# Optimization experiments

Hardware: AMD Instinct MI355X
Metric: run time of the kernel (lower is better)

The kernel has to match this reference:

```python
import jax, jax.numpy as jnp
import numpy as np


def _unfold(x, k, pad, stride):
    # torch.nn.functional.unfold: [B,C,H,W] -> [B, C*k*k, L]
    B, C, H, W = x.shape
    xp = jnp.pad(x, ((0, 0), (0, 0), (pad, pad), (pad, pad)))
    Ho = (H + 2 * pad - k) // stride + 1
    Wo = (W + 2 * pad - k) // stride + 1
    ih = stride * jnp.arange(Ho)[:, None] + jnp.arange(k)[None, :]  # [Ho,k]
    iw = stride * jnp.arange(Wo)[:, None] + jnp.arange(k)[None, :]  # [Wo,k]
    p = xp[:, :, ih][:, :, :, :, iw]          # [B,C,Ho,k,Wo,k]
    p = p.transpose(0, 1, 3, 5, 2, 4)          # [B,C,k,k,Ho,Wo]
    return p.reshape(B, C * k * k, Ho * Wo)


def _fold(cols, out_hw, k, pad, stride):
    # torch.nn.functional.fold (col2im, overlap-add)
    B, D, L = cols.shape
    C = D // (k * k)
    Ho = (out_hw[0] + 2 * pad - k) // stride + 1
    Wo = (out_hw[1] + 2 * pad - k) // stride + 1
    x = cols.reshape(B, C, k, k, Ho, Wo).transpose(0, 1, 2, 4, 3, 5)  # [B,C,k,Ho,k,Wo]
    ih = stride * jnp.arange(Ho)[None, :] + jnp.arange(k)[:, None]    # [k,Ho]
    iw = stride * jnp.arange(Wo)[None, :] + jnp.arange(k)[:, None]    # [k,Wo]
    out = jnp.zeros((B, C, out_hw[0] + 2 * pad, out_hw[1] + 2 * pad), cols.dtype)
    out = out.at[:, :, ih[:, :, None, None], iw[None, None, :, :]].add(x)
    return out[:, :, pad:pad + out_hw[0], pad:pad + out_hw[1]]


def _l2norm(x, axis):
    # torch F.normalize with eps=1e-12 (clamp_min on the norm)
    n = jnp.sqrt(jnp.sum(x * x, axis=axis, keepdims=True))
    return x / jnp.clip(n, 1e-12)


def _cubic(x):
    # PyTorch bicubic kernel, a=-0.75
    a = -0.75
    ax = jnp.abs(x)
    ax2 = ax * ax
    ax3 = ax2 * ax
    w1 = (a + 2.0) * ax3 - (a + 3.0) * ax2 + 1.0
    w2 = a * ax3 - 5.0 * a * ax2 + 8.0 * a * ax - 4.0 * a
    return jnp.where(ax <= 1.0, w1, jnp.where(ax < 2.0, w2, 0.0))


def _upsample1d_bicubic(x, axis, scale):
    # align_corners=False: src = (dst+0.5)/scale - 0.5, border-replicated 4-tap
    n = x.shape[axis]
    out = jnp.arange(n * scale, dtype=jnp.float32)
    src = (out + 0.5) / scale - 0.5
    f = jnp.floor(src)
    t = src - f
    offs = jnp.arange(-1, 3)
    idx = jnp.clip(f[:, None].astype(jnp.int32) + offs[None, :], 0, n - 1)   # [No,4]
    w = _cubic(t[:, None] - offs[None, :].astype(jnp.float32))               # [No,4]
    g = jnp.take(x, idx, axis=axis)  # inserts dims (No,4) at `axis`
    w_shape = [1] * g.ndim
    w_shape[axis] = idx.shape[0]
    w_shape[axis + 1] = 4
    return jnp.sum(g * w.reshape(w_shape), axis=axis + 1)


def _bicubic(R, scale):
    # R: [B, N_ref, N_lr] treated as a 1-channel image, upscale both axes
    R = _upsample1d_bicubic(R, 1, scale)
    return _upsample1d_bicubic(R, 2, scale)


def setup_inputs() -> dict:
    key = jax.random.key(0)
    ks = jax.random.split(key, 9)
    shapes = {
        'lrsr_lv1': (2, 256, 16, 16), 'lrsr_lv2': (2, 128, 32, 32), 'lrsr_lv3': (2, 64, 64, 64),
        'refsr_lv1': (2, 256, 16, 16), 'refsr_lv2': (2, 128, 32, 32), 'refsr_lv3': (2, 64, 64, 64),
        'ref_lv1': (2, 64, 256, 256), 'ref_lv2': (2, 128, 128, 128), 'ref_lv3': (2, 256, 64, 64),
    }
    return {name: jax.random.normal(k, shp, dtype=jnp.float32)
            for k, (name, shp) in zip(ks, shapes.items())}


def reference(lrsr_lv1, lrsr_lv2, lrsr_lv3, refsr_lv1, refsr_lv2, refsr_lv3, ref_lv1, ref_lv2, ref_lv3):
    # unfold + L2-normalize descriptors
    l3 = _l2norm(_unfold(lrsr_lv3, 3, 1, 1), 1)   # [B, D3, N3]
    l2 = _l2norm(_unfold(lrsr_lv2, 3, 1, 1), 1)
    l1 = _l2norm(_unfold(lrsr_lv1, 3, 1, 1), 1)
    r3 = _l2norm(jnp.swapaxes(_unfold(refsr_lv3, 3, 1, 1), 1, 2), 2)  # [B, N3, D3]
    r2 = _l2norm(jnp.swapaxes(_unfold(refsr_lv2, 3, 1, 1), 1, 2), 2)
    r1 = _l2norm(jnp.swapaxes(_unfold(refsr_lv1, 3, 1, 1), 1, 2), 2)
    # cosine correlation per scale
    R3 = jnp.einsum('bnd,bdm->bnm', r3, l3)   # [B, N3, N3]
    R2 = jnp.einsum('bnd,bdm->bnm', r2, l2)   # [B, N3/4, N3/4]
    R1 = jnp.einsum('bnd,bdm->bnm', r1, l1)   # [B, N3/16, N3/16]
    R = (R3 + _bicubic(R2, 4) + _bicubic(R1, 16)) / 3.0
    star = jnp.max(R, axis=1)                 # [B, N3]
    arg = jnp.argmax(R, axis=1)               # [B, N3]
    # retrieval gather on reference patches
    u3 = _unfold(ref_lv3, 3, 1, 1)
    u2 = _unfold(ref_lv2, 6, 2, 2)
    u1 = _unfold(ref_lv1, 12, 4, 4)
    gather = lambda u: jnp.take_along_axis(u, arg[:, None, :], axis=2)
    B = lrsr_lv3.shape[0]
    H, W = lrsr_lv3.shape[2], lrsr_lv3.shape[3]
    T_lv3 = _fold(gather(u3), (H, W), 3, 1, 1) / 9.0
    T_lv2 = _fold(gather(u2), (2 * H, 2 * W), 6, 2, 2) / 9.0
    T_lv1 = _fold(gather(u1), (4 * H, 4 * W), 12, 4, 4) / 9.0
    S_3 = star.reshape(B, 1, H, W)
    return (S_3, T_lv3, T_lv2, T_lv1)
```

## Files before the change

### kernel.cpp

```cpp
#include <hip/hip_runtime.h>
#include <cstdint>

#define DIVUP(a,b) (((a)+(b)-1)/(b))

typedef __attribute__((ext_vector_type(4))) float f32x4;
typedef __attribute__((ext_vector_type(8))) _Float16 half8;

__device__ __forceinline__ void gload_lds16(const void* g, void* l) {
  __builtin_amdgcn_global_load_lds(
      (const __attribute__((address_space(1))) void*)g,
      (__attribute__((address_space(3))) void*)l, 16, 0, 0);
}

__device__ __forceinline__ float cubicw(float x) {
  float ax = fabsf(x);
  float ax2 = ax * ax;
  float ax3 = ax2 * ax;
  if (ax <= 1.0f) return 1.25f * ax3 - 2.25f * ax2 + 1.0f;
  if (ax < 2.0f)  return -0.75f * ax3 + 3.75f * ax2 - 6.0f * ax + 3.0f;
  return 0.0f;
}

__global__ void sumsq_multi(const float* __restrict__ r3, const float* __restrict__ l3,
                            const float* __restrict__ r2, const float* __restrict__ l2,
                            const float* __restrict__ r1, const float* __restrict__ l1,
                            float* __restrict__ S) {
  int blk = blockIdx.x;
  const float* x; int C, HW, so, base;
  if (blk < 32)      { x = r3; C = 64;  HW = 4096; so = 0;     base = 0;  }
  else if (blk < 64) { x = l3; C = 64;  HW = 4096; so = 8192;  base = 32; }
  else if (blk < 72) { x = r2; C = 128; HW = 1024; so = 16384; base = 64; }
  else if (blk < 80) { x = l2; C = 128; HW = 1024; so = 18432; base = 72; }
  else if (blk < 82) { x = r1; C = 256; HW = 256;  so = 20480; base = 80; }
  else               { x = l1; C = 256; HW = 256;  so = 20992; base = 82; }
  int i = (blk - base) * 256 + threadIdx.x;
  if (i >= 2 * HW) return;
  int pix = i % HW, b = i / HW;
  const float* p = x + (size_t)b * C * HW + pix;
  float s = 0.f;
  for (int c = 0; c < C; ++c) { float v = p[(size_t)c * HW]; s += v * v; }
  S[so + i] = s;
}

__global__ void invnorm_multi(const float* __restrict__ S, float* __restrict__ invn) {
  int blk = blockIdx.x;
  int H, so, base;
  if (blk < 32)      { H = 64; so = 0;     base = 0;  }
  else if (blk < 64) { H = 64; so = 8192;  base = 32; }
  else if (blk < 72) { H = 32; so = 16384; base = 64; }
  else if (blk < 80) { H = 32; so = 18432; base = 72; }
  else if (blk < 82) { H = 16; so = 20480; base = 80; }
  else               { H = 16; so = 20992; base = 82; }
  int W = H;
  int i = (blk - base) * 256 + threadIdx.x;
  if (i >= 2 * H * W) return;
  int p = i % (H * W), b = i / (H * W);
  int ph = p / W, pw = p % W;
  const float* Sb = S + so + (size_t)b * H * W;
  float s = 0.f;
  for (int ki = 0; ki < 3; ++ki) {
    int y = ph + ki - 1;
    if (y < 0 || y >= H) continue;
    for (int kj = 0; kj < 3; ++kj) {
      int xx = pw + kj - 1;
      if (xx < 0 || xx >= W) continue;
      s += Sb[y * W + xx];
    }
  }
  float n = fmaxf(sqrtf(s), 1e-12f);
  invn[so + i] = 1.0f / n;
}

__global__ void desc_split_multi(const float* __restrict__ r3, const float* __restrict__ l3,
                                 _Float16* __restrict__ r3hi, _Float16* __restrict__ r3lo,
                                 _Float16* __restrict__ l3hi, _Float16* __restrict__ l3lo,
                                 const float* __restrict__ invn) {
  const int C = 64, H = 64, W = 64;
  int blk = blockIdx.x;
  int job = blk >> 11;
  const float* x = job ? l3 : r3;
  _Float16* hi = job ? l3hi : r3hi;
  _Float16* lo = job ? l3lo : r3lo;
  int io = job ? 8192 : 0;
  int i = (blk & 2047) * 256 + threadIdx.x;
  if (i >= 2 * C * H * W) return;
  int c = i % C;
  int p = (i / C) % (H * W);
  int b = i / (C * H * W);
  int ph = p / W, pw = p % W;
  float s = invn[io + b * H * W + p];
  size_t obase = ((size_t)b * H * W + p) * (size_t)(C * 9) + (size_t)c * 9;
  const float* xb = x + (size_t)(b * C + c) * H * W;
#pragma unroll
  for (int r = 0; r < 9; ++r) {
    int y = ph + r / 3 - 1, xx = pw + r % 3 - 1;
    float v = 0.f;
    if (y >= 0 && y < H && xx >= 0 && xx < W) v = xb[y * W + xx] * s;
    _Float16 h = (_Float16)v;
    float hf = (float)h;
    _Float16 l = (_Float16)((v - hf) * 4096.0f);
    hi[obase + r] = h;
    lo[obase + r] = l;
  }
}

__global__ void desc_l_multi(const float* __restrict__ l2in, const float* __restrict__ l1in,
                             float* __restrict__ l2n, float* __restrict__ l1n,
                             const float* __restrict__ invn) {
  int blk = blockIdx.x;
  const float* x; float* out; int C, H, io, base;
  if (blk < 9216) { x = l2in; out = l2n; C = 128; H = 32; io = 18432; base = 0; }
  else            { x = l1in; out = l1n; C = 256; H = 16; io = 20992; base = 9216; }
  int W = H, HW = H * W, D = C * 9;
  int i = (blk - base) * 256 + threadIdx.x;
  if (i >= 2 * D * HW) return;
  int p = i % HW;
  int d = (i / HW) % D;
  int b = i / (HW * D);
  int c = d / 9, r = d % 9, ki = r / 3, kj = r % 3;
  int ph = p / W, pw = p % W;
  int y = ph + ki - 1, xx = pw + kj - 1;
  float v = 0.f;
  if (y >= 0 && y < H && xx >= 0 && xx < W) v = x[((size_t)(b * C + c) * H + y) * W + xx];
  out[i] = v * invn[io + b * HW + p];
}

__global__ void desc_r_multi(const float* __restrict__ r2in, const float* __restrict__ r1in,
                             float* __restrict__ r2n, float* __restrict__ r1n,
                             const float* __restrict__ invn) {
  int blk = blockIdx.x;
  const float* x; float* out; int C, H, io, base;
  if (blk < 9216) { x = r2in; out = r2n; C = 128; H = 32; io = 16384; base = 0; }
  else            { x = r1in; out = r1n; C = 256; H = 16; io = 20480; base = 9216; }
  int W = H, HW = H * W, D = C * 9;
  int i = (blk - base) * 256 + threadIdx.x;
  if (i >= 2 * D * HW) return;
  int d = i % D;
  int p = (i / D) % HW;
  int b = i / (D * HW);
  int c = d / 9, r = d % 9, ki = r / 3, kj = r % 3;
  int ph = p / W, pw = p % W;
  int y = ph + ki - 1, xx = pw + kj - 1;
  float v = 0.f;
  if (y >= 0 && y < H && xx >= 0 && xx < W) v = x[((size_t)(b * C + c) * H + y) * W + xx];
  out[i] = v * invn[io + b * HW + p];
}

__global__ void upsample_multi(const float* __restrict__ R2, const float* __restrict__ R1,
                               float* __restrict__ up2, float* __restrict__ up1) {
  int blk = blockIdx.x;
  const float* Rin; float* out; int Nin, cols, base; float invscale;
  if (blk < 32768) { Rin = R2; out = up2; Nin = 1024; cols = 1024; invscale = 0.25f;   base = 0; }
  else             { Rin = R1; out = up1; Nin = 256;  cols = 256;  invscale = 0.0625f; base = 32768; }
  int i = (blk - base) * 256 + threadIdx.x;
  if (i >= 2 * 4096 * cols) return;
  int j = i % cols;
  int n = (i / cols) & 4095;
  int b = i / (cols * 4096);
  float src = (n + 0.5f) * invscale - 0.5f;
  float f = floorf(src);
  float tt = src - f;
  int fi = (int)f;
  const float* Rb = Rin + (size_t)b * Nin * cols;
  float s = 0.f;
#pragma unroll
  for (int tp = 0; tp < 4; ++tp) {
    int ii = min(max(fi + tp - 1, 0), Nin - 1);
    s += cubicw(tt - (float)(tp - 1)) * Rb[(size_t)ii * cols + j];
  }
  out[i] = s;
}

__global__ void init_multi(unsigned long long* __restrict__ R1z,
                           unsigned long long* __restrict__ pk) {
  int i = blockIdx.x * blockDim.x + threadIdx.x;
  if (i < 65536) R1z[i] = 0ull;
  else if (i < 65536 + 8192) pk[i - 65536] = 0ull;
}

__global__ __launch_bounds__(256)
void gemm64_kernel(const float* __restrict__ A, const float* __restrict__ B,
                   float* __restrict__ C, int M, int N, int K) {
  int b = blockIdx.z;
  const float* Ab = A + (size_t)b * M * K;
  const float* Bb = B + (size_t)b * K * N;
  __shared__ float As[16][68];
  __shared__ float Bs[16][64];
  int row0 = blockIdx.y * 64;
  int col0 = blockIdx.x * 64;
  int t = threadIdx.x;
  int tx = t & 15, ty = t >> 4;
  float acc[4][4] = {};
  int la_r = t >> 2;
  int la_k = (t & 3) << 2;
  int lb_r = t >> 4;
  int lb_c = (t & 15) << 2;
  const float* Aptr = Ab + (size_t)(row0 + la_r) * K + la_k;
  const float* Bptr = Bb + (size_t)lb_r * N + col0 + lb_c;
  float4 av = *(const float4*)(Aptr);
  float4 bv = *(const float4*)(Bptr);
  for (int k0 = 0; k0 < K; k0 += 16) {
    __syncthreads();
    As[la_k + 0][la_r] = av.x;
    As[la_k + 1][la_r] = av.y;
    As[la_k + 2][la_r] = av.z;
    As[la_k + 3][la_r] = av.w;
    *(float4*)&Bs[lb_r][lb_c] = bv;
    __syncthreads();
    if (k0 + 16 < K) {
      av = *(const float4*)(Aptr + k0 + 16);
      bv = *(const float4*)(Bptr + (size_t)(k0 + 16) * N);
    }
#pragma unroll
    for (int k = 0; k < 16; ++k) {
      float4 a = *(const float4*)&As[k][ty << 2];
      float4 bq = *(const float4*)&Bs[k][tx << 2];
      float av4[4] = {a.x, a.y, a.z, a.w};
      float bv4[4] = {bq.x, bq.y, bq.z, bq.w};
#pragma unroll
      for (int ii = 0; ii < 4; ++ii)
#pragma unroll
        for (int jj = 0; jj < 4; ++jj)
          acc[ii][jj] = fmaf(av4[ii], bv4[jj], acc[ii][jj]);
    }
  }
  float* Cb = C + (size_t)b * M * N;
#pragma unroll
  for (int ii = 0; ii < 4; ++ii) {
    float4 v = make_float4(acc[ii][0], acc[ii][1], acc[ii][2], acc[ii][3]);
    *(float4*)&Cb[(size_t)(row0 + (ty << 2) + ii) * N + col0 + (tx << 2)] = v;
  }
}

__global__ __launch_bounds__(256)
void gemm64sk_kernel(const float* __restrict__ A, const float* __restrict__ B,
                     float* __restrict__ C, int M, int N, int K, int SK) {
  int zz = blockIdx.z;
  int b = zz / SK, kc = zz % SK;
  int kchunk = K / SK;
  int kbeg = kc * kchunk, kend = kbeg + kchunk;
  const float* Ab = A + (size_t)b * M * K;
  const float* Bb = B + (size_t)b * K * N;
  __shared__ float As[16][68];
  __shared__ float Bs[16][64];
  int row0 = blockIdx.y * 64;
  int col0 = blockIdx.x * 64;
  int t = threadIdx.x;
  int tx = t & 15, ty = t >> 4;
  float acc[4][4] = {};
  int la_r = t >> 2;
  int la_k = (t & 3) << 2;
  int lb_r = t >> 4;
  int lb_c = (t & 15) << 2;
  const float* Aptr = Ab + (size_t)(row0 + la_r) * K + la_k;
  const float* Bptr = Bb + (size_t)lb_r * N + col0 + lb_c;
  float4 av = *(const float4*)(Aptr + kbeg);
  float4 bv = *(const float4*)(Bptr + (size_t)kbeg * N);
  for (int k0 = kbeg; k0 < kend; k0 += 16) {
    __syncthreads();
    As[la_k + 0][la_r] = av.x;
    As[la_k + 1][la_r] = av.y;
    As[la_k + 2][la_r] = av.z;
    As[la_k + 3][la_r] = av.w;
    *(float4*)&Bs[lb_r][lb_c] = bv;
    __syncthreads();
    if (k0 + 16 < kend) {
      av = *(const float4*)(Aptr + k0 + 16);
      bv = *(const float4*)(Bptr + (size_t)(k0 + 16) * N);
    }
#pragma unroll
    for (int k = 0; k < 16; ++k) {
      float4 a = *(const float4*)&As[k][ty << 2];
      float4 bq = *(const float4*)&Bs[k][tx << 2];
      float av4[4] = {a.x, a.y, a.z, a.w};
      float bv4[4] = {bq.x, bq.y, bq.z, bq.w};
#pragma unroll
      for (int ii = 0; ii < 4; ++ii)
#pragma unroll
        for (int jj = 0; jj < 4; ++jj)
          acc[ii][jj] = fmaf(av4[ii], bv4[jj], acc[ii][jj]);
    }
  }
  float* Cb = C + (size_t)b * M * N;
#pragma unroll
  for (int ii = 0; ii < 4; ++ii)
#pragma unroll
    for (int jj = 0; jj < 4; ++jj)
      atomicAdd(&Cb[(size_t)(row0 + (ty << 2) + ii) * N + col0 + (tx << 2) + jj],
                acc[ii][jj]);
}

__global__ __launch_bounds__(256, 2)
void mfma_fused_kernel(const _Float16* __restrict__ Ahi, const _Float16* __restrict__ Alo,
                       const _Float16* __restrict__ Bhi, const _Float16* __restrict__ Blo,
                       const float* __restrict__ up2, const float* __restrict__ up1,
                       unsigned long long* __restrict__ packed) {
  const int K = 576;
  int bid = (blockIdx.z * 32 + blockIdx.y) * 32 + blockIdx.x;
  int swz = (bid & 7) * 256 + (bid >> 3);
  int bx = swz & 31;
  int by = (swz >> 5) & 31;
  int b  = swz >> 10;

  int row0 = by * 128;
  int col0 = bx * 128;
  int t = threadIdx.x;
  int lane = t & 63, wave = t >> 6;
  int wy = wave & 1, wx = wave >> 1;
  int quad = lane >> 4, lm = lane & 15;

  __shared__ _Float16 lds[2 * 4 * 4096];

  int off[2];
#pragma unroll
  for (int h = 0; h < 2; ++h) {
    int d = wave * 128 + h * 64 + lane;
    int line = d >> 3;
    int c3 = (d & 7) ^ (line & 7);
    int row = (line << 1) | (c3 >> 2);
    int c = c3 & 3;
    off[h] = row * (K * 2) + c * 16;
  }
  const char* pg[4];
  pg[0] = (const char*)Ahi + ((size_t)b * 4096 + row0) * (size_t)K * 2;
  pg[1] = (const char*)Alo + ((size_t)b * 4096 + row0) * (size_t)K * 2;
  pg[2] = (const char*)Bhi + ((size_t)b * 4096 + col0) * (size_t)K * 2;
  pg[3] = (const char*)Blo + ((size_t)b * 4096 + col0) * (size_t)K * 2;

  int ra[4], rb[4];
#pragma unroll
  for (int i = 0; i < 4; ++i) {
    int rowa = wy * 64 + i * 16 + lm;
    int la_ = rowa >> 1;
    ra[i] = la_ * 128 + (((((rowa & 1) << 2) | quad) ^ (la_ & 7)) << 4);
    int rowb = wx * 64 + i * 16 + lm;
    int lb_ = rowb >> 1;
    rb[i] = lb_ * 128 + (((((rowb & 1) << 2) | quad) ^ (lb_ & 7)) << 4);
  }

  f32x4 S1[4][4] = {};
  f32x4 S2[4][4] = {};

#pragma unroll
  for (int p = 0; p < 4; ++p) {
    char* lb_ = (char*)lds + p * 8192 + wave * 2048;
    gload_lds16(pg[p] + off[0], lb_);
    gload_lds16(pg[p] + off[1], lb_ + 1024);
  }
  __syncthreads();

  int buf = 0;
  for (int t18 = 0; t18 < 18; ++t18) {
    const char* lb = (const char*)lds + buf * 32768;
    half8 aH[4], aL[4], bH[4], bL[4];
#pragma unroll
    for (int i = 0; i < 4; ++i) {
      aH[i] = *(const half8*)(lb + ra[i]);
      aL[i] = *(const half8*)(lb + 8192 + ra[i]);
      bH[i] = *(const half8*)(lb + 16384 + rb[i]);
      bL[i] = *(const half8*)(lb + 24576 + rb[i]);
    }
    if (t18 < 17) {
      int kbyte = (t18 + 1) * 64;
#pragma unroll
      for (int p = 0; p < 4; ++p) {
        char* lw = (char*)lds + (buf ^ 1) * 32768 + p * 8192 + wave * 2048;
        gload_lds16(pg[p] + kbyte + off[0], lw);
        gload_lds16(pg[p] + kbyte + off[1], lw + 1024);
      }
    }
#pragma unroll
    for (int i = 0; i < 4; ++i)
#pragma unroll
      for (int j = 0; j < 4; ++j) {
        S1[i][j] = __builtin_amdgcn_mfma_f32_16x16x32_f16(aH[i], bH[j], S1[i][j], 0, 0, 0);
        S2[i][j] = __builtin_amdgcn_mfma_f32_16x16x32_f16(aH[i], bL[j], S2[i][j], 0, 0, 0);
        S2[i][j] = __builtin_amdgcn_mfma_f32_16x16x32_f16(aL[i], bH[j], S2[i][j], 0, 0, 0);
      }
    __syncthreads();
    buf ^= 1;
  }

  const float inv4096 = 1.0f / 4096.0f;
  const float* u2b = up2 + (size_t)b * 4096 * 1024;
  const float* u1b = up1 + (size_t)b * 4096 * 256;
#pragma unroll
  for (int j = 0; j < 4; ++j) {
    int gm = col0 + wx * 64 + j * 16 + lm;
    float src2 = (gm + 0.5f) * 0.25f - 0.5f;
    float f2 = floorf(src2); float t2 = src2 - f2; int i2 = (int)f2;
    int idx2[4]; float w2[4];
#pragma unroll
    for (int tp = 0; tp < 4; ++tp) {
      idx2[tp] = min(max(i2 + tp - 1, 0), 1023);
      w2[tp] = cubicw(t2 - (float)(tp - 1));
    }
    float src1 = (gm + 0.5f) * 0.0625f - 0.5f;
    float f1 = floorf(src1); float t1 = src1 - f1; int i1 = (int)f1;
    int idx1[4]; float w1[4];
#pragma unroll
    for (int tp = 0; tp < 4; ++tp) {
      idx1[tp] = min(max(i1 + tp - 1, 0), 255);
      w1[tp] = cubicw(t1 - (float)(tp - 1));
    }
    unsigned long long best = 0ull;
#pragma unroll
    for (int i = 0; i < 4; ++i) {
#pragma unroll
      for (int r = 0; r < 4; ++r) {
        int gn = row0 + wy * 64 + i * 16 + quad * 4 + r;
        float v = S1[i][j][r] + S2[i][j][r] * inv4096;
        const float* r2row = u2b + (size_t)gn * 1024;
        const float* r1row = u1b + (size_t)gn * 256;
        v += w2[0] * r2row[idx2[0]] + w2[1] * r2row[idx2[1]]
           + w2[2] * r2row[idx2[2]] + w2[3] * r2row[idx2[3]];
        v += w1[0] * r1row[idx1[0]] + w1[1] * r1row[idx1[1]]
           + w1[2] * r1row[idx1[2]] + w1[3] * r1row[idx1[3]];
        v *= (1.0f / 3.0f);
        unsigned int fb = __float_as_uint(v);
        unsigned int key = (fb & 0x80000000u) ? ~fb : (fb | 0x80000000u);
        unsigned long long pk = ((unsigned long long)key << 32)
                              | (unsigned long long)(0xFFFFFFFFu - (unsigned)gn);
        best = best > pk ? best : pk;
      }
    }
    unsigned long long o;
    o = __shfl_xor(best, 16); best = best > o ? best : o;
    o = __shfl_xor(best, 32); best = best > o ? best : o;
    if (lane < 16) atomicMax(&packed[(size_t)b * 4096 + gm], best);
  }
}

__global__ void finalize_kernel(const unsigned long long* __restrict__ packed,
                                float* __restrict__ s3_out, int* __restrict__ arg, int total) {
  int i = blockIdx.x * blockDim.x + threadIdx.x;
  if (i >= total) return;
  unsigned long long pk = packed[i];
  unsigned int key = (unsigned int)(pk >> 32);
  unsigned int fb = (key & 0x80000000u) ? (key ^ 0x80000000u) : ~key;
  s3_out[i] = __uint_as_float(fb);
  arg[i] = (int)(0xFFFFFFFFu - (unsigned int)(pk & 0xFFFFFFFFull));
}

__global__ __launch_bounds__(256)
void transpose_multi(const float* __restrict__ ref3, const float* __restrict__ ref2,
                     const float* __restrict__ ref1, float* __restrict__ o3,
                     float* __restrict__ o2, float* __restrict__ o1) {
  __shared__ float tile[32][33];
  int blk = blockIdx.x;
  const float* in; float* out; int R, S, gx, gy, base;
  if (blk < 2048)      { in = ref3; out = o3; R = 256; S = 4096;  gx = 128;  gy = 8; base = 0; }
  else if (blk < 6144) { in = ref2; out = o2; R = 128; S = 16384; gx = 512;  gy = 4; base = 2048; }
  else                 { in = ref1; out = o1; R = 64;  S = 65536; gx = 2048; gy = 2; base = 6144; }
  int local = blk - base;
  int pb = gx * gy;
  int b = local / pb;
  int rem = local % pb;
  int r0 = (rem / gx) * 32;
  int s0 = (rem % gx) * 32;
  int tx = threadIdx.x & 31, ty = threadIdx.x >> 5;
  const float* ib = in + (size_t)b * R * S;
  float* ob = out + (size_t)b * R * S;
#pragma unroll
  for (int k = 0; k < 4; ++k)
    tile[ty + 8 * k][tx] = ib[(size_t)(r0 + ty + 8 * k) * S + s0 + tx];
  __syncthreads();
#pragma unroll
  for (int k = 0; k < 4; ++k)
    ob[(size_t)(s0 + ty + 8 * k) * R + r0 + tx] = tile[tx][ty + 8 * k];
}

template<int KK, int SS, int PP, int CL2, int WL2>
__global__ __launch_bounds__(256)
void foldT_kernel(const float* __restrict__ refT, const int* __restrict__ arg,
                  float* __restrict__ outCF) {
  const int C = 1 << CL2, W = 1 << WL2;
  const int NK = (C / 4) / 16;
  __shared__ float lds[C * 17];
  int tid = threadIdx.x;
  int pl = tid >> 4, c4g = tid & 15;
  int w0 = blockIdx.x * 16;
  int h = blockIdx.y;
  int b = blockIdx.z;
  int w = w0 + pl;
  int y = h + PP, x = w + PP;
  int ho_lo = (y - KK + 1) > 0 ? (y - KK + 1 + SS - 1) / SS : 0;
  int ho_hi = min(63, y / SS);
  int wo_lo = (x - KK + 1) > 0 ? (x - KK + 1 + SS - 1) / SS : 0;
  int wo_hi = min(63, x / SS);
  const int* argb = arg + b * 4096;
  const f32x4* refb4 = (const f32x4*)(refT + ((size_t)b << (2 * WL2 + CL2)));
  f32x4 acc[NK] = {};
  for (int ho = ho_lo; ho <= ho_hi; ++ho) {
    int ki = y - SS * ho;
    for (int wo = wo_lo; wo <= wo_hi; ++wo) {
      int kj = x - SS * wo;
      int q = argb[(ho << 6) + wo];
      int qh = q >> 6, qw = q & 63;
      int ry = SS * qh + ki - PP;
      int rx = SS * qw + kj - PP;
      if (ry >= 0 && ry < W && rx >= 0 && rx < W) {
        const f32x4* pb4 = refb4 + (((size_t)(ry << WL2) + rx) << (CL2 - 2));
#pragma unroll
        for (int k = 0; k < NK; ++k) acc[k] += pb4[c4g + k * 16];
      }
    }
  }
#pragma unroll
  for (int k = 0; k < NK; ++k) {
    int c4 = c4g + k * 16;
#pragma unroll
    for (int j = 0; j < 4; ++j)
      lds[(4 * c4 + j) * 17 + pl] = acc[k][j] * (1.0f / 9.0f);
  }
  __syncthreads();
  size_t ob = ((size_t)(b * C)) << (2 * WL2);
  for (int idx = tid; idx < C * 16; idx += 256) {
    int c = idx >> 4, j = idx & 15;
    outCF[ob + ((size_t)c << (2 * WL2)) + (h << WL2) + w0 + j] = lds[c * 17 + j];
  }
}

extern "C" void kernel_launch(void* const* d_in, const int* in_sizes, int n_in,
                              void* d_out, int out_size, void* d_ws, size_t ws_size,
                              hipStream_t stream) {
  const float* lrsr1 = (const float*)d_in[0];
  const float* lrsr2 = (const float*)d_in[1];
  const float* lrsr3 = (const float*)d_in[2];
  const float* refsr1 = (const float*)d_in[3];
  const float* refsr2 = (const float*)d_in[4];
  const float* refsr3 = (const float*)d_in[5];
  const float* ref1 = (const float*)d_in[6];
  const float* ref2 = (const float*)d_in[7];
  const float* ref3 = (const float*)d_in[8];
  float* out = (float*)d_out;
  float* ws = (float*)d_ws;

  const int B = 2;
  size_t off_planes = 0;
  size_t off_r2n = off_planes + (size_t)B * 4096 * 576 * 2;
  size_t off_l2n = off_r2n + (size_t)B * 1024 * 1152;
  size_t off_r1n = off_l2n + (size_t)B * 1152 * 1024;
  size_t off_l1n = off_r1n + (size_t)B * 256 * 2304;
  size_t off_R2  = off_l1n + (size_t)B * 2304 * 256;
  size_t off_R1  = off_R2  + (size_t)B * 1024 * 1024;
  size_t off_up2 = off_R1  + (size_t)B * 256 * 256;
  size_t off_up1 = off_up2 + (size_t)B * 4096 * 1024;
  size_t off_S   = off_up1 + (size_t)B * 4096 * 256;
  size_t off_invn= off_S   + 21504;
  size_t off_pk  = off_invn+ 21504;
  size_t off_arg = off_pk  + (size_t)B * 4096 * 2;

  const size_t PLANE = (size_t)B * 4096 * 576;
  _Float16* r3hi = (_Float16*)(ws + off_planes);
  _Float16* r3lo = r3hi + PLANE;
  _Float16* l3hi = r3lo + PLANE;
  _Float16* l3lo = l3hi + PLANE;

  unsigned long long* pk = (unsigned long long*)(ws + off_pk);
  int* argp = (int*)(ws + off_arg);

  init_multi<<<288, 256, 0, stream>>>((unsigned long long*)(ws + off_R1), pk);
  sumsq_multi<<<84, 256, 0, stream>>>(refsr3, lrsr3, refsr2, lrsr2, refsr1, lrsr1,
                                      ws + off_S);
  invnorm_multi<<<84, 256, 0, stream>>>(ws + off_S, ws + off_invn);
  desc_split_multi<<<4096, 256, 0, stream>>>(refsr3, lrsr3, r3hi, r3lo, l3hi, l3lo,
                                             ws + off_invn);
  desc_l_multi<<<13824, 256, 0, stream>>>(lrsr2, lrsr1, ws + off_l2n, ws + off_l1n,
                                          ws + off_invn);
  desc_r_multi<<<13824, 256, 0, stream>>>(refsr2, refsr1, ws + off_r2n, ws + off_r1n,
                                          ws + off_invn);
  {
    dim3 g(1024 / 64, 1024 / 64, B);
    gemm64_kernel<<<g, 256, 0, stream>>>(ws + off_r2n, ws + off_l2n, ws + off_R2,
                                         1024, 1024, 1152);
  }
  {
    dim3 g(256 / 64, 256 / 64, B * 8);
    gemm64sk_kernel<<<g, 256, 0, stream>>>(ws + off_r1n, ws + off_l1n, ws + off_R1,
                                           256, 256, 2304, 8);
  }
  upsample_multi<<<40960, 256, 0, stream>>>(ws + off_R2, ws + off_R1,
                                            ws + off_up2, ws + off_up1);
  {
    dim3 g(4096 / 128, 4096 / 128, B);
    mfma_fused_kernel<<<g, 256, 0, stream>>>(r3hi, r3lo, l3hi, l3lo,
                                             ws + off_up2, ws + off_up1, pk);
  }
  finalize_kernel<<<DIVUP(B * 4096, 256), 256, 0, stream>>>(pk, out, argp, B * 4096);

  float* refT3 = ws + off_planes;
  float* refT2 = refT3 + (size_t)2 * 256 * 4096;
  float* refT1 = ws + off_up2;
  transpose_multi<<<14336, 256, 0, stream>>>(ref3, ref2, ref1, refT3, refT2, refT1);

  float* T3 = out + 8192;
  float* T2 = T3 + (size_t)B * 256 * 64 * 64;
  float* T1 = T2 + (size_t)B * 128 * 128 * 128;
  {
    dim3 g(64 / 16, 64, B);
    foldT_kernel<3, 1, 1, 8, 6><<<g, 256, 0, stream>>>(refT3, argp, T3);
  }
  {
    dim3 g(128 / 16, 128, B);
    foldT_kernel<6, 2, 2, 7, 7><<<g, 256, 0, stream>>>(refT2, argp, T2);
  }
  {
    dim3 g(256 / 16, 256, B);
    foldT_kernel<12, 4, 4, 6, 8><<<g, 256, 0, stream>>>(refT1, argp, T1);
  }
}
```

Measured before the change: 664.0 us.

## Move level-2 correlation GEMM to split-fp16 MFMA and merge fold launches

Replaces the fp32 SIMT GEMM for the level-2 correlation with an MFMA kernel that uses hi/lo fp16 split operands, as the level-3 path already does. The level-2 descriptors are now produced by the split descriptor kernel in a [N,D] fp16 layout instead of normalized fp32. The three fold launches are merged into one dispatch with a shared body. This targets the FMA-bound fp32 GEMM and some launch overhead, at the cost of extra split-plane memory and the small precision loss of the three-product split.

Result: faster. 639.5 us (-3.7%).

```diff
diff --git a/kernel.cpp b/kernel.cpp
--- a/kernel.cpp
+++ b/kernel.cpp
@@ -72,25 +72,28 @@
 }
 
 __global__ void desc_split_multi(const float* __restrict__ r3, const float* __restrict__ l3,
+                                 const float* __restrict__ r2, const float* __restrict__ l2,
                                  _Float16* __restrict__ r3hi, _Float16* __restrict__ r3lo,
                                  _Float16* __restrict__ l3hi, _Float16* __restrict__ l3lo,
+                                 _Float16* __restrict__ r2hi, _Float16* __restrict__ r2lo,
+                                 _Float16* __restrict__ l2hi, _Float16* __restrict__ l2lo,
                                  const float* __restrict__ invn) {
-  const int C = 64, H = 64, W = 64;
   int blk = blockIdx.x;
-  int job = blk >> 11;
-  const float* x = job ? l3 : r3;
-  _Float16* hi = job ? l3hi : r3hi;
-  _Float16* lo = job ? l3lo : r3lo;
-  int io = job ? 8192 : 0;
-  int i = (blk & 2047) * 256 + threadIdx.x;
-  if (i >= 2 * C * H * W) return;
+  const float* x; _Float16* hi; _Float16* lo; int C, H, io, base;
+  if (blk < 2048)      { x = r3; hi = r3hi; lo = r3lo; C = 64;  H = 64; io = 0;     base = 0; }
+  else if (blk < 4096) { x = l3; hi = l3hi; lo = l3lo; C = 64;  H = 64; io = 8192;  base = 2048; }
+  else if (blk < 5120) { x = r2; hi = r2hi; lo = r2lo; C = 128; H = 32; io = 16384; base = 4096; }
+  else                 { x = l2; hi = l2hi; lo = l2lo; C = 128; H = 32; io = 18432; base = 5120; }
+  int W = H, HW = H * W;
+  int i = (blk - base) * 256 + threadIdx.x;
+  if (i >= 2 * C * HW) return;
   int c = i % C;
-  int p = (i / C) % (H * W);
-  int b = i / (C * H * W);
+  int p = (i / C) % HW;
+  int b = i / (C * HW);
   int ph = p / W, pw = p % W;
-  float s = invn[io + b * H * W + p];
-  size_t obase = ((size_t)b * H * W + p) * (size_t)(C * 9) + (size_t)c * 9;
-  const float* xb = x + (size_t)(b * C + c) * H * W;
+  float s = invn[io + b * HW + p];
+  size_t obase = ((size_t)b * HW + p) * (size_t)(C * 9) + (size_t)c * 9;
+  const float* xb = x + (size_t)(b * C + c) * HW;
 #pragma unroll
   for (int r = 0; r < 9; ++r) {
     int y = ph + r / 3 - 1, xx = pw + r % 3 - 1;
@@ -104,15 +107,10 @@
   }
 }
 
-__global__ void desc_l_multi(const float* __restrict__ l2in, const float* __restrict__ l1in,
-                             float* __restrict__ l2n, float* __restrict__ l1n,
-                             const float* __restrict__ invn) {
-  int blk = blockIdx.x;
-  const float* x; float* out; int C, H, io, base;
-  if (blk < 9216) { x = l2in; out = l2n; C = 128; H = 32; io = 18432; base = 0; }
-  else            { x = l1in; out = l1n; C = 256; H = 16; io = 20992; base = 9216; }
-  int W = H, HW = H * W, D = C * 9;
-  int i = (blk - base) * 256 + threadIdx.x;
+__global__ void desc_l1_kernel(const float* __restrict__ x, float* __restrict__ out,
+                               const float* __restrict__ invn) {
+  const int C = 256, H = 16, W = 16, HW = 256, D = 2304, io = 20992;
+  int i = blockIdx.x * 256 + threadIdx.x;
   if (i >= 2 * D * HW) return;
   int p = i % HW;
   int d = (i / HW) % D;
@@ -125,15 +123,10 @@
   out[i] = v * invn[io + b * HW + p];
 }
 
-__global__ void desc_r_multi(const float* __restrict__ r2in, const float* __restrict__ r1in,
-                             float* __restrict__ r2n, float* __restrict__ r1n,
-                             const float* __restrict__ invn) {
-  int blk = blockIdx.x;
-  const float* x; float* out; int C, H, io, base;
-  if (blk < 9216) { x = r2in; out = r2n; C = 128; H = 32; io = 16384; base = 0; }
-  else            { x = r1in; out = r1n; C = 256; H = 16; io = 20480; base = 9216; }
-  int W = H, HW = H * W, D = C * 9;
-  int i = (blk - base) * 256 + threadIdx.x;
+__global__ void desc_r1_kernel(const float* __restrict__ x, float* __restrict__ out,
+                               const float* __restrict__ invn) {
+  const int C = 256, H = 16, W = 16, HW = 256, D = 2304, io = 20480;
+  int i = blockIdx.x * 256 + threadIdx.x;
   if (i >= 2 * D * HW) return;
   int d = i % D;
   int p = (i / D) % HW;
@@ -176,60 +169,6 @@
   int i = blockIdx.x * blockDim.x + threadIdx.x;
   if (i < 65536) R1z[i] = 0ull;
   else if (i < 65536 + 8192) pk[i - 65536] = 0ull;
-}
-
-__global__ __launch_bounds__(256)
-void gemm64_kernel(const float* __restrict__ A, const float* __restrict__ B,
-                   float* __restrict__ C, int M, int N, int K) {
-  int b = blockIdx.z;
-  const float* Ab = A + (size_t)b * M * K;
-  const float* Bb = B + (size_t)b * K * N;
-  __shared__ float As[16][68];
-  __shared__ float Bs[16][64];
-  int row0 = blockIdx.y * 64;
-  int col0 = blockIdx.x * 64;
-  int t = threadIdx.x;
-  int tx = t & 15, ty = t >> 4;
-  float acc[4][4] = {};
-  int la_r = t >> 2;
-  int la_k = (t & 3) << 2;
-  int lb_r = t >> 4;
-  int lb_c = (t & 15) << 2;
-  const float* Aptr = Ab + (size_t)(row0 + la_r) * K + la_k;
-  const float* Bptr = Bb + (size_t)lb_r * N + col0 + lb_c;
-  float4 av = *(const float4*)(Aptr);
-  float4 bv = *(const float4*)(Bptr);
-  for (int k0 = 0; k0 < K; k0 += 16) {
-    __syncthreads();
-    As[la_k + 0][la_r] = av.x;
-    As[la_k + 1][la_r] = av.y;
-    As[la_k + 2][la_r] = av.z;
-    As[la_k + 3][la_r] = av.w;
-    *(float4*)&Bs[lb_r][lb_c] = bv;
-    __syncthreads();
-    if (k0 + 16 < K) {
-      av = *(const float4*)(Aptr + k0 + 16);
-      bv = *(const float4*)(Bptr + (size_t)(k0 + 16) * N);
-    }
-#pragma unroll
-    for (int k = 0; k < 16; ++k) {
-      float4 a = *(const float4*)&As[k][ty << 2];
-      float4 bq = *(const float4*)&Bs[k][tx << 2];
-      float av4[4] = {a.x, a.y, a.z, a.w};
-      float bv4[4] = {bq.x, bq.y, bq.z, bq.w};
-#pragma unroll
-      for (int ii = 0; ii < 4; ++ii)
-#pragma unroll
-        for (int jj = 0; jj < 4; ++jj)
-          acc[ii][jj] = fmaf(av4[ii], bv4[jj], acc[ii][jj]);
-    }
-  }
-  float* Cb = C + (size_t)b * M * N;
-#pragma unroll
-  for (int ii = 0; ii < 4; ++ii) {
-    float4 v = make_float4(acc[ii][0], acc[ii][1], acc[ii][2], acc[ii][3]);
-    *(float4*)&Cb[(size_t)(row0 + (ty << 2) + ii) * N + col0 + (tx << 2)] = v;
-  }
 }
 
 __global__ __launch_bounds__(256)
@@ -291,6 +230,105 @@
 }
 
 __global__ __launch_bounds__(256, 2)
+void mfma_r2_kernel(const _Float16* __restrict__ Ahi, const _Float16* __restrict__ Alo,
+                    const _Float16* __restrict__ Bhi, const _Float16* __restrict__ Blo,
+                    float* __restrict__ Cout) {
+  const int K = 1152;
+  int bx = blockIdx.x, by = blockIdx.y, b = blockIdx.z;
+  int row0 = by * 128;
+  int col0 = bx * 128;
+  int t = threadIdx.x;
+  int lane = t & 63, wave = t >> 6;
+  int wy = wave & 1, wx = wave >> 1;
+  int quad = lane >> 4, lm = lane & 15;
+
+  __shared__ _Float16 lds[2 * 4 * 4096];
+
+  int off[2];
+#pragma unroll
+  for (int h = 0; h < 2; ++h) {
+    int d = wave * 128 + h * 64 + lane;
+    int line = d >> 3;
+    int c3 = (d & 7) ^ (line & 7);
+    int row = (line << 1) | (c3 >> 2);
+    int c = c3 & 3;
+    off[h] = row * (K * 2) + c * 16;
+  }
+  const char* pg[4];
+  pg[0] = (const char*)Ahi + ((size_t)b * 1024 + row0) * (size_t)K * 2;
+  pg[1] = (const char*)Alo + ((size_t)b * 1024 + row0) * (size_t)K * 2;
+  pg[2] = (const char*)Bhi + ((size_t)b * 1024 + col0) * (size_t)K * 2;
+  pg[3] = (const char*)Blo + ((size_t)b * 1024 + col0) * (size_t)K * 2;
+
+  int ra[4], rb[4];
+#pragma unroll
+  for (int i = 0; i < 4; ++i) {
+    int rowa = wy * 64 + i * 16 + lm;
+    int la_ = rowa >> 1;
+    ra[i] = la_ * 128 + (((((rowa & 1) << 2) | quad) ^ (la_ & 7)) << 4);
+    int rowb = wx * 64 + i * 16 + lm;
+    int lb_ = rowb >> 1;
+    rb[i] = lb_ * 128 + (((((rowb & 1) << 2) | quad) ^ (lb_ & 7)) << 4);
+  }
+
+  f32x4 S1[4][4] = {};
+  f32x4 S2[4][4] = {};
+
+#pragma unroll
+  for (int p = 0; p < 4; ++p) {
+    char* lb_ = (char*)lds + p * 8192 + wave * 2048;
+    gload_lds16(pg[p] + off[0], lb_);
+    gload_lds16(pg[p] + off[1], lb_ + 1024);
+  }
+  __syncthreads();
+
+  int buf = 0;
+  for (int tki = 0; tki < 36; ++tki) {
+    const char* lb = (const char*)lds + buf * 32768;
+    half8 aH[4], aL[4], bH[4], bL[4];
+#pragma unroll
+    for (int i = 0; i < 4; ++i) {
+      aH[i] = *(const half8*)(lb + ra[i]);
+      aL[i] = *(const half8*)(lb + 8192 + ra[i]);
+      bH[i] = *(const half8*)(lb + 16384 + rb[i]);
+      bL[i] = *(const half8*)(lb + 24576 + rb[i]);
+    }
+    if (tki < 35) {
+      int kbyte = (tki + 1) * 64;
+#pragma unroll
+      for (int p = 0; p < 4; ++p) {
+        char* lw = (char*)lds + (buf ^ 1) * 32768 + p * 8192 + wave * 2048;
+        gload_lds16(pg[p] + kbyte + off[0], lw);
+        gload_lds16(pg[p] + kbyte + off[1], lw + 1024);
+      }
+    }
+#pragma unroll
+    for (int i = 0; i < 4; ++i)
+#pragma unroll
+      for (int j = 0; j < 4; ++j) {
+        S1[i][j] = __builtin_amdgcn_mfma_f32_16x16x32_f16(aH[i], bH[j], S1[i][j], 0, 0, 0);
+        S2[i][j] = __builtin_amdgcn_mfma_f32_16x16x32_f16(aH[i], bL[j], S2[i][j], 0, 0, 0);
+        S2[i][j] = __builtin_amdgcn_mfma_f32_16x16x32_f16(aL[i], bH[j], S2[i][j], 0, 0, 0);
+      }
+    __syncthreads();
+    buf ^= 1;
+  }
+
+  const float inv4096 = 1.0f / 4096.0f;
+  float* Cb = Cout + (size_t)b * 1024 * 1024;
+#pragma unroll
+  for (int i = 0; i < 4; ++i)
+#pragma unroll
+    for (int j = 0; j < 4; ++j)
+#pragma unroll
+      for (int r = 0; r < 4; ++r) {
+        int gn = row0 + wy * 64 + i * 16 + quad * 4 + r;
+        int gm = col0 + wx * 64 + j * 16 + lm;
+        Cb[(size_t)gn * 1024 + gm] = S1[i][j][r] + S2[i][j][r] * inv4096;
+      }
+}
+
+__global__ __launch_bounds__(256, 2)
 void mfma_fused_kernel(const _Float16* __restrict__ Ahi, const _Float16* __restrict__ Alo,
                        const _Float16* __restrict__ Bhi, const _Float16* __restrict__ Blo,
                        const float* __restrict__ up2, const float* __restrict__ up1,
@@ -471,17 +509,15 @@
 }
 
 template<int KK, int SS, int PP, int CL2, int WL2>
-__global__ __launch_bounds__(256)
-void foldT_kernel(const float* __restrict__ refT, const int* __restrict__ arg,
-                  float* __restrict__ outCF) {
+__device__ __forceinline__ void foldT_body(const float* __restrict__ refT,
+                                           const int* __restrict__ arg,
+                                           float* __restrict__ outCF,
+                                           float* lds, int bx, int h, int b) {
   const int C = 1 << CL2, W = 1 << WL2;
   const int NK = (C / 4) / 16;
-  __shared__ float lds[C * 17];
   int tid = threadIdx.x;
   int pl = tid >> 4, c4g = tid & 15;
-  int w0 = blockIdx.x * 16;
-  int h = blockIdx.y;
-  int b = blockIdx.z;
+  int w0 = bx * 16;
   int w = w0 + pl;
   int y = h + PP, x = w + PP;
   int ho_lo = (y - KK + 1) > 0 ? (y - KK + 1 + SS - 1) / SS : 0;
@@ -521,6 +557,24 @@
   }
 }
 
+__global__ __launch_bounds__(256)
+void foldT_all(const float* __restrict__ refT3, const float* __restrict__ refT2,
+               const float* __restrict__ refT1, const int* __restrict__ arg,
+               float* __restrict__ T3, float* __restrict__ T2, float* __restrict__ T1) {
+  __shared__ float lds[256 * 17];
+  int blk = blockIdx.x;
+  if (blk < 512) {
+    int local = blk;
+    foldT_body<3, 1, 1, 8, 6>(refT3, arg, T3, lds, local & 3, (local >> 2) & 63, local >> 8);
+  } else if (blk < 2560) {
+    int local = blk - 512;
+    foldT_body<6, 2, 2, 7, 7>(refT2, arg, T2, lds, local & 7, (local >> 3) & 127, local >> 10);
+  } else {
+    int local = blk - 2560;
+    foldT_body<12, 4, 4, 6, 8>(refT1, arg, T1, lds, local & 15, (local >> 4) & 255, local >> 12);
+  }
+}
+
 extern "C" void kernel_launch(void* const* d_in, const int* in_sizes, int n_in,
                               void* d_out, int out_size, void* d_ws, size_t ws_size,
                               hipStream_t stream) {
@@ -538,9 +592,8 @@
 
   const int B = 2;
   size_t off_planes = 0;
-  size_t off_r2n = off_planes + (size_t)B * 4096 * 576 * 2;
-  size_t off_l2n = off_r2n + (size_t)B * 1024 * 1152;
-  size_t off_r1n = off_l2n + (size_t)B * 1152 * 1024;
+  size_t off_pl2 = off_planes + (size_t)B * 4096 * 576 * 2;
+  size_t off_r1n = off_pl2 + (size_t)B * 1024 * 1152 * 2;
   size_t off_l1n = off_r1n + (size_t)B * 256 * 2304;
   size_t off_R2  = off_l1n + (size_t)B * 2304 * 256;
   size_t off_R1  = off_R2  + (size_t)B * 1024 * 1024;
@@ -551,11 +604,16 @@
   size_t off_pk  = off_invn+ 21504;
   size_t off_arg = off_pk  + (size_t)B * 4096 * 2;
 
-  const size_t PLANE = (size_t)B * 4096 * 576;
+  const size_t PLANE3 = (size_t)B * 4096 * 576;
   _Float16* r3hi = (_Float16*)(ws + off_planes);
-  _Float16* r3lo = r3hi + PLANE;
-  _Float16* l3hi = r3lo + PLANE;
-  _Float16* l3lo = l3hi + PLANE;
+  _Float16* r3lo = r3hi + PLANE3;
+  _Float16* l3hi = r3lo + PLANE3;
+  _Float16* l3lo = l3hi + PLANE3;
+  const size_t PLANE2 = (size_t)B * 1024 * 1152;
+  _Float16* r2hi = (_Float16*)(ws + off_pl2);
+  _Float16* r2lo = r2hi + PLANE2;
+  _Float16* l2hi = r2lo + PLANE2;
+  _Float16* l2lo = l2hi + PLANE2;
 
   unsigned long long* pk = (unsigned long long*)(ws + off_pk);
   int* argp = (int*)(ws + off_arg);
@@ -564,16 +622,15 @@
   sumsq_multi<<<84, 256, 0, stream>>>(refsr3, lrsr3, refsr2, lrsr2, refsr1, lrsr1,
                                       ws + off_S);
   invnorm_multi<<<84, 256, 0, stream>>>(ws + off_S, ws + off_invn);
-  desc_split_multi<<<4096, 256, 0, stream>>>(refsr3, lrsr3, r3hi, r3lo, l3hi, l3lo,
+  desc_split_multi<<<6144, 256, 0, stream>>>(refsr3, lrsr3, refsr2, lrsr2,
+                                             r3hi, r3lo, l3hi, l3lo,
+                                             r2hi, r2lo, l2hi, l2lo,
                                              ws + off_invn);
-  desc_l_multi<<<13824, 256, 0, stream>>>(lrsr2, lrsr1, ws + off_l2n, ws + off_l1n,
-                                          ws + off_invn);
-  desc_r_multi<<<13824, 256, 0, stream>>>(refsr2, refsr1, ws + off_r2n, ws + off_r1n,
-                                          ws + off_invn);
+  desc_l1_kernel<<<4608, 256, 0, stream>>>(lrsr1, ws + off_l1n, ws + off_invn);
+  desc_r1_kernel<<<4608, 256, 0, stream>>>(refsr1, ws + off_r1n, ws + off_invn);
   {
-    dim3 g(1024 / 64, 1024 / 64, B);
-    gemm64_kernel<<<g, 256, 0, stream>>>(ws + off_r2n, ws + off_l2n, ws + off_R2,
-                                         1024, 1024, 1152);
+    dim3 g(8, 8, B);
+    mfma_r2_kernel<<<g, 256, 0, stream>>>(r2hi, r2lo, l2hi, l2lo, ws + off_R2);
   }
   {
     dim3 g(256 / 64, 256 / 64, B * 8);
@@ -597,16 +654,5 @@
   float* T3 = out + 8192;
   float* T2 = T3 + (size_t)B * 256 * 64 * 64;
   float* T1 = T2 + (size_t)B * 128 * 128 * 128;
-  {
-    dim3 g(64 / 16, 64, B);
-    foldT_kernel<3, 1, 1, 8, 6><<<g, 256, 0, stream>>>(refT3, argp, T3);
-  }
-  {
-    dim3 g(128 / 16, 128, B);
-    foldT_kernel<6, 2, 2, 7, 7><<<g, 256, 0, stream>>>(refT2, argp, T2);
-  }
-  {
-    dim3 g(256 / 16, 256, B);
-    foldT_kernel<12, 4, 4, 6, 8><<<g, 256, 0, stream>>>(refT1, argp, T1);
-  }
-}
+  foldT_all<<<10752, 256, 0, stream>>>(refT3, refT2, refT1, argp, T3, T2, T1);
+}
```
